# Kernel optimization log

Measured on AMD Instinct MI355X. Metric: run time of the kernel, lower is better.

## Reference

```python
import jax, jax.numpy as jnp
import numpy as np

SIGMA = 1.0


def _pairwise_max(q, fact_emb):
    # q: [B, N, D], fact_emb: [F, D]  (D = 3E)
    # Gaussian RBF kernel k(x,y) = exp(-||x-y||^2 / (2*sigma^2)), then max over F.
    q2 = jnp.sum(q * q, axis=-1, keepdims=True)            # [B, N, 1]
    f2 = jnp.sum(fact_emb * fact_emb, axis=-1)             # [F]
    qf = jnp.einsum('bnd,fd->bnf', q, fact_emb)            # [B, N, F]
    d2 = jnp.maximum(q2 + f2[None, None, :] - 2.0 * qf, 0.0)
    k = jnp.exp(-d2 / (2.0 * SIGMA ** 2))                  # [B, N, F]
    return jnp.max(k, axis=2)                              # [B, N]


def setup_inputs() -> dict:
    key = jax.random.key(0)
    ks = jax.random.split(key, 7)
    B, N, F, E = 8, 4000, 4000, 100
    return {
        'rel': jax.random.normal(ks[0], (B, E), jnp.float32),
        'arg1': jax.random.normal(ks[1], (B, E), jnp.float32),
        'arg2': jax.random.normal(ks[2], (B, E), jnp.float32),
        'fact_rel': jax.random.normal(ks[3], (F, E), jnp.float32),
        'fact_arg1': jax.random.normal(ks[4], (F, E), jnp.float32),
        'fact_arg2': jax.random.normal(ks[5], (F, E), jnp.float32),
        'entity_embeddings': jax.random.normal(ks[6], (N, E), jnp.float32),
    }


def reference(rel, arg1, arg2, fact_rel, fact_arg1, fact_arg2, entity_embeddings):
    B = rel.shape[0]
    N, E = entity_embeddings.shape
    fact_emb = jnp.concatenate([fact_rel, fact_arg1, fact_arg2], axis=1)  # [F, 3E]

    rel_b = jnp.broadcast_to(rel[:, None, :], (B, N, E))
    emb_b = jnp.broadcast_to(entity_embeddings[None, :, :], (B, N, E))

    # score_sp: query = [rel, arg1, entity]
    arg1_b = jnp.broadcast_to(arg1[:, None, :], (B, N, E))
    q_sp = jnp.concatenate([rel_b, arg1_b, emb_b], axis=2)  # [B, N, 3E]
    score_sp = _pairwise_max(q_sp, fact_emb)                # [B, N]

    # score_po: query = [rel, entity, arg2]
    arg2_b = jnp.broadcast_to(arg2[:, None, :], (B, N, E))
    q_po = jnp.concatenate([rel_b, emb_b, arg2_b], axis=2)  # [B, N, 3E]
    score_po = _pairwise_max(q_po, fact_emb)                # [B, N]

    return (score_sp, score_po)
```

## Files before the change

### kernel.cpp

```cpp
#include <hip/hip_runtime.h>
#include <math.h>

#define EDIM 100
#define KP   128
#define NF   4000
#define NN   4000
#define NB   8
#define NP   4096
#define BN   128
#define BF   64
#define FPB  4
#define NYB  16

#define CONVB (3 * NP * 16 / 256)
#define PREPB ((NP / 64) * NB)
#define E2B   ((NN + 255) / 256)

typedef __attribute__((ext_vector_type(8))) short short8;
typedef __attribute__((ext_vector_type(4))) float floatx4;

__device__ __align__(16) unsigned short g_A [NP * KP];
__device__ __align__(16) unsigned short g_B1[NP * KP];
__device__ __align__(16) unsigned short g_B2[NP * KP];
__device__ __align__(16) float g_P[2 * NB * NP];
__device__ float g_e2[NN];
__device__ float g_part[2 * NB * NYB * NP];

__device__ __forceinline__ unsigned short f2bf(float x) {
    union { float f; unsigned int u; } v; v.f = x;
    unsigned int r = v.u + 0x7FFFu + ((v.u >> 16) & 1u);
    return (unsigned short)(r >> 16);
}

__device__ __forceinline__ float row16_min(float x) {
    int i;
    i = __builtin_amdgcn_mov_dpp(__float_as_int(x), 0x140, 0xF, 0xF, false);
    x = fminf(x, __int_as_float(i));
    i = __builtin_amdgcn_mov_dpp(__float_as_int(x), 0x141, 0xF, 0xF, false);
    x = fminf(x, __int_as_float(i));
    i = __builtin_amdgcn_mov_dpp(__float_as_int(x), 0x1B, 0xF, 0xF, false);
    x = fminf(x, __int_as_float(i));
    i = __builtin_amdgcn_mov_dpp(__float_as_int(x), 0xB1, 0xF, 0xF, false);
    x = fminf(x, __int_as_float(i));
    return x;
}

__global__ void prep(const float* __restrict__ rel,  const float* __restrict__ arg1,
                     const float* __restrict__ arg2, const float* __restrict__ frel,
                     const float* __restrict__ fa1,  const float* __restrict__ fa2,
                     const float* __restrict__ ent) {
    const int bx = blockIdx.x;
    const int t  = threadIdx.x;

    if (bx < CONVB) {
        int plane = bx >> 8;
        int local = ((bx & 255) << 8) | t;
        int row = local >> 4, j = local & 15;
        const float* src = (plane == 0) ? ent : (plane == 1) ? fa1 : fa2;
        unsigned short* dst = (plane == 0) ? g_A : (plane == 1) ? g_B1 : g_B2;
        short8 o = (short8){0, 0, 0, 0, 0, 0, 0, 0};
        if (row < NF && j <= 12) {
            if (j < 12) {
                float4 v0 = *(const float4*)(src + row * EDIM + j * 8);
                float4 v1 = *(const float4*)(src + row * EDIM + j * 8 + 4);
                o[0] = (short)f2bf(v0.x); o[1] = (short)f2bf(v0.y);
                o[2] = (short)f2bf(v0.z); o[3] = (short)f2bf(v0.w);
                o[4] = (short)f2bf(v1.x); o[5] = (short)f2bf(v1.y);
                o[6] = (short)f2bf(v1.z); o[7] = (short)f2bf(v1.w);
            } else {
                float4 v0 = *(const float4*)(src + row * EDIM + 96);
                o[0] = (short)f2bf(v0.x); o[1] = (short)f2bf(v0.y);
                o[2] = (short)f2bf(v0.z); o[3] = (short)f2bf(v0.w);
            }
        }
        *(short8*)(dst + row * KP + j * 8) = o;
    } else if (bx < CONVB + PREPB) {
        int pb = bx - CONVB;
        int b   = pb >> 6;
        int fbx = pb & 63;
        int lane = t & 63;
        int wv = t >> 6;
        int fl = lane & 15;
        int kq = lane >> 4;
        int f = fbx * 64 + wv * 16 + fl;
        int fr = (f < NF) ? f : (NF - 1);

        float nf = 0.f, dr = 0.f, d1 = 0.f, d2 = 0.f, qr = 0.f, q1 = 0.f, q2 = 0.f;
        for (int i = 0; i < 25; i++) {
            int k = kq * 25 + i;
            float vr = frel[fr * EDIM + k];
            float v1 = fa1[fr * EDIM + k];
            float v2 = fa2[fr * EDIM + k];
            float rb = rel[b * EDIM + k];
            float a1 = arg1[b * EDIM + k];
            float a2 = arg2[b * EDIM + k];
            nf += vr * vr + v1 * v1 + v2 * v2;
            dr = fmaf(rb, vr, dr);
            d1 = fmaf(a1, v1, d1);
            d2 = fmaf(a2, v2, d2);
            qr = fmaf(rb, rb, qr);
            q1 = fmaf(a1, a1, q1);
            q2 = fmaf(a2, a2, q2);
        }
        nf += __shfl_xor(nf, 16); nf += __shfl_xor(nf, 32);
        dr += __shfl_xor(dr, 16); dr += __shfl_xor(dr, 32);
        d1 += __shfl_xor(d1, 16); d1 += __shfl_xor(d1, 32);
        d2 += __shfl_xor(d2, 16); d2 += __shfl_xor(d2, 32);
        qr += __shfl_xor(qr, 16); qr += __shfl_xor(qr, 32);
        q1 += __shfl_xor(q1, 16); q1 += __shfl_xor(q1, 32);
        q2 += __shfl_xor(q2, 16); q2 += __shfl_xor(q2, 32);
        if (kq == 0) {
            float psp = nf + qr + q1 - 2.f * (dr + d1);
            float ppo = nf + qr + q2 - 2.f * (dr + d2);
            if (f >= NF) { psp = __builtin_inff(); ppo = __builtin_inff(); }
            g_P[(0 * NB + b) * NP + f] = psp;
            g_P[(1 * NB + b) * NP + f] = ppo;
        }
    } else {
        int n = (bx - CONVB - PREPB) * 256 + t;
        if (n < NN) {
            const float4* ep = (const float4*)(ent + n * EDIM);
            float s = 0.f;
            #pragma unroll
            for (int i = 0; i < EDIM / 4; i++) {
                float4 v = ep[i];
                s += v.x * v.x + v.y * v.y + v.z * v.z + v.w * v.w;
            }
            g_e2[n] = s;
        }
    }
}

__global__ void __launch_bounds__(256, 2) main_kernel() {
    __shared__ float4 smem4[4352];
    float4* lA4  = smem4;
    float4* lB14 = smem4 + 2048;
    float4* lB24 = smem4 + 3072;
    float*  sPf  = (float*)(smem4 + 4096);

    const int t = threadIdx.x;
    const int n0 = blockIdx.x * BN;
    const int by = blockIdx.y;
    const int lane = t & 63;
    const int c = lane & 15;
    const int q = lane >> 4;
    const int w = t >> 6;
    const int w32 = w * 32;

    floatx4 m2[2][8][2];
    #pragma unroll
    for (int g = 0; g < 2; g++)
        #pragma unroll
        for (int b = 0; b < NB; b++)
            #pragma unroll
            for (int mt = 0; mt < 2; mt++)
                m2[g][b][mt] = (floatx4){__builtin_inff(), __builtin_inff(),
                                         __builtin_inff(), __builtin_inff()};

    const float4* gA4  = (const float4*)g_A;
    const float4* gB14 = (const float4*)g_B1;
    const float4* gB24 = (const float4*)g_B2;

    #pragma unroll
    for (int i = 0; i < 8; i++) {
        int gc = i * 256 + t;
        int rw = gc >> 4, ch = gc & 15;
        lA4[rw * 16 + (ch ^ (rw & 15))] = gA4[n0 * 16 + gc];
    }

    #pragma unroll 1
    for (int ib = 0; ib < FPB; ib++) {
        const int f0 = (by * FPB + ib) * BF;

        #pragma unroll
        for (int i = 0; i < 4; i++) {
            int gc = i * 256 + t;
            int rw = gc >> 4, ch = gc & 15;
            int sl = rw * 16 + (ch ^ (rw & 15));
            lB14[sl] = gB14[f0 * 16 + gc];
            lB24[sl] = gB24[f0 * 16 + gc];
        }
        {
            int pg = t >> 7, pb = (t >> 4) & 7, q4 = t & 15;
            ((float4*)sPf)[t] = ((const float4*)(g_P + (pg * NB + pb) * NP + f0))[q4];
        }
        __syncthreads();

        const short8* pA  = (const short8*)lA4;
        const short8* pB1 = (const short8*)lB14;
        const short8* pB2 = (const short8*)lB24;

        #pragma unroll
        for (int g = 0; g < 2; g++) {
            const short8* pB = g ? pB1 : pB2;
            floatx4 acc[2][4];
            #pragma unroll
            for (int mt = 0; mt < 2; mt++)
                #pragma unroll
                for (int ft = 0; ft < 4; ft++)
                    acc[mt][ft] = (floatx4){0.f, 0.f, 0.f, 0.f};

            #pragma unroll
            for (int s = 0; s < 4; s++) {
                const int base = s * 4 + q;
                short8 a0 = pA[(w32 + c) * 16 + (base ^ c)];
                short8 a1 = pA[(w32 + 16 + c) * 16 + (base ^ c)];
                #pragma unroll
                for (int ft = 0; ft < 4; ft++) {
                    short8 bb = pB[(ft * 16 + c) * 16 + (base ^ c)];
                    acc[0][ft] = __builtin_amdgcn_mfma_f32_16x16x32_bf16(a0, bb, acc[0][ft], 0, 0, 0);
                    acc[1][ft] = __builtin_amdgcn_mfma_f32_16x16x32_bf16(a1, bb, acc[1][ft], 0, 0, 0);
                }
            }

            #pragma unroll
            for (int b = 0; b < NB; b++) {
                const float* Pb = sPf + (g * NB + b) * 64;
                float p0 = Pb[c];
                float p1 = Pb[16 + c];
                float p2 = Pb[32 + c];
                float p3 = Pb[48 + c];
                #pragma unroll
                for (int mt = 0; mt < 2; mt++) {
                    #pragma unroll
                    for (int r = 0; r < 4; r++) {
                        float t0 = fmaf(-2.f, acc[mt][0][r], p0);
                        float t1 = fmaf(-2.f, acc[mt][1][r], p1);
                        float t2 = fmaf(-2.f, acc[mt][2][r], p2);
                        float t3 = fmaf(-2.f, acc[mt][3][r], p3);
                        float u = fminf(fminf(t0, t1), t2);
                        m2[g][b][mt][r] = fminf(fminf(u, t3), m2[g][b][mt][r]);
                    }
                }
            }
        }
        if (ib < FPB - 1) __syncthreads();
    }

    #pragma unroll
    for (int g = 0; g < 2; g++)
        #pragma unroll
        for (int b = 0; b < NB; b++)
            #pragma unroll
            for (int mt = 0; mt < 2; mt++)
                #pragma unroll
                for (int r = 0; r < 4; r++)
                    m2[g][b][mt][r] = row16_min(m2[g][b][mt][r]);

    if (c == 0) {
        #pragma unroll
        for (int g = 0; g < 2; g++)
            #pragma unroll
            for (int b = 0; b < NB; b++)
                #pragma unroll
                for (int mt = 0; mt < 2; mt++)
                    *(float4*)&g_part[((g * NB + b) * NYB + by) * NP +
                                      n0 + w32 + mt * 16 + q * 4] =
                        (float4){m2[g][b][mt][0], m2[g][b][mt][1],
                                 m2[g][b][mt][2], m2[g][b][mt][3]};
    }
}

__global__ void finalize(float* __restrict__ out) {
    int idx = blockIdx.x * 256 + threadIdx.x;
    if (idx >= 2 * NB * NN) return;
    int sb = idx / NN;
    int n = idx % NN;
    float m = __builtin_inff();
    #pragma unroll
    for (int j = 0; j < NYB; j += 2) {
        float a = g_part[(sb * NYB + j) * NP + n];
        float b = g_part[(sb * NYB + j + 1) * NP + n];
        m = fminf(m, fminf(a, b));
    }
    float d2 = fmaxf(m + g_e2[n], 0.f);
    out[idx] = expf(-0.5f * d2);
}

extern "C" void kernel_launch(void* const* d_in, const int* in_sizes, int n_in,
                              void* d_out, int out_size, void* d_ws, size_t ws_size,
                              hipStream_t stream) {
    const float* rel  = (const float*)d_in[0];
    const float* arg1 = (const float*)d_in[1];
    const float* arg2 = (const float*)d_in[2];
    const float* frel = (const float*)d_in[3];
    const float* fa1  = (const float*)d_in[4];
    const float* fa2  = (const float*)d_in[5];
    const float* ent  = (const float*)d_in[6];
    float* out = (float*)d_out;

    prep<<<dim3(CONVB + PREPB + E2B), 256, 0, stream>>>(rel, arg1, arg2, frel, fa1, fa2, ent);
    main_kernel<<<dim3(NP / BN, NYB), 256, 0, stream>>>();
    finalize<<<(2 * NB * NN + 255) / 256, 256, 0, stream>>>(out);
}
```

Baseline: 127.4 us.

## Split query groups across grid z, keep A in registers, double-buffer B via direct LDS loads

Adds a grid z dimension so each block handles only one of the two score groups, which halves the per-thread min accumulators. The A fragments are loaded straight into registers instead of shared memory. B tiles and the P vectors are double-buffered in LDS using global_load_lds, so the next tile's load overlaps the current MFMA work. P is reordered in the prep kernel into a swizzled layout so each lane reads one float4 per batch. This doubles the block count and re-reads A per group, in exchange for lower register pressure and fewer synchronisation stalls.

```diff
diff --git a/kernel.cpp b/kernel.cpp
--- a/kernel.cpp
+++ b/kernel.cpp
@@ -19,10 +19,13 @@
 typedef __attribute__((ext_vector_type(8))) short short8;
 typedef __attribute__((ext_vector_type(4))) float floatx4;
 
+typedef const __attribute__((address_space(1))) unsigned int* gas_u32;
+typedef __attribute__((address_space(3))) unsigned int* las_u32;
+
 __device__ __align__(16) unsigned short g_A [NP * KP];
 __device__ __align__(16) unsigned short g_B1[NP * KP];
 __device__ __align__(16) unsigned short g_B2[NP * KP];
-__device__ __align__(16) float g_P[2 * NB * NP];
+__device__ __align__(16) float g_P2[2 * 64 * 512];
 __device__ float g_e2[NN];
 __device__ float g_part[2 * NB * NYB * NP];
 
@@ -113,8 +116,12 @@
             float psp = nf + qr + q1 - 2.f * (dr + d1);
             float ppo = nf + qr + q2 - 2.f * (dr + d2);
             if (f >= NF) { psp = __builtin_inff(); ppo = __builtin_inff(); }
-            g_P[(0 * NB + b) * NP + f] = psp;
-            g_P[(1 * NB + b) * NP + f] = ppo;
+            int fblk = f >> 6;
+            int cc = f & 15;
+            int ft = (f & 63) >> 4;
+            int chunk = cc * 8 + (b ^ (cc & 7));
+            g_P2[(0 * 64 + fblk) * 512 + chunk * 4 + ft] = psp;
+            g_P2[(1 * 64 + fblk) * 512 + chunk * 4 + ft] = ppo;
         }
     } else {
         int n = (bx - CONVB - PREPB) * 256 + t;
@@ -132,132 +139,118 @@
 }
 
 __global__ void __launch_bounds__(256, 2) main_kernel() {
-    __shared__ float4 smem4[4352];
-    float4* lA4  = smem4;
-    float4* lB14 = smem4 + 2048;
-    float4* lB24 = smem4 + 3072;
-    float*  sPf  = (float*)(smem4 + 4096);
+    __shared__ __align__(16) unsigned short sB[2][BF * 128];
+    __shared__ __align__(16) float sP[2][512];
 
     const int t = threadIdx.x;
     const int n0 = blockIdx.x * BN;
     const int by = blockIdx.y;
+    const int g  = blockIdx.z;
     const int lane = t & 63;
     const int c = lane & 15;
     const int q = lane >> 4;
     const int w = t >> 6;
     const int w32 = w * 32;
 
-    floatx4 m2[2][8][2];
-    #pragma unroll
-    for (int g = 0; g < 2; g++)
-        #pragma unroll
-        for (int b = 0; b < NB; b++)
-            #pragma unroll
-            for (int mt = 0; mt < 2; mt++)
-                m2[g][b][mt] = (floatx4){__builtin_inff(), __builtin_inff(),
-                                         __builtin_inff(), __builtin_inff()};
-
-    const float4* gA4  = (const float4*)g_A;
-    const float4* gB14 = (const float4*)g_B1;
-    const float4* gB24 = (const float4*)g_B2;
-
-    #pragma unroll
-    for (int i = 0; i < 8; i++) {
-        int gc = i * 256 + t;
-        int rw = gc >> 4, ch = gc & 15;
-        lA4[rw * 16 + (ch ^ (rw & 15))] = gA4[n0 * 16 + gc];
-    }
+    const unsigned short* gB = g ? g_B1 : g_B2;
+
+    short8 afrag[2][4];
+    #pragma unroll
+    for (int mt = 0; mt < 2; mt++)
+        #pragma unroll
+        for (int s = 0; s < 4; s++)
+            afrag[mt][s] = *(const short8*)(g_A + (n0 + w32 + mt * 16 + c) * KP + (s * 4 + q) * 8);
+
+    floatx4 m2[NB][2];
+    #pragma unroll
+    for (int b = 0; b < NB; b++)
+        #pragma unroll
+        for (int mt = 0; mt < 2; mt++)
+            m2[b][mt] = (floatx4){__builtin_inff(), __builtin_inff(),
+                                  __builtin_inff(), __builtin_inff()};
+
+    auto stage = [&](int buf, int fb) {
+        const int f0r = fb * BF;
+        #pragma unroll
+        for (int j = 0; j < 4; j++) {
+            int ck = (w * 4 + j) * 64 + lane;
+            int rw = ck >> 4, ch = ck & 15;
+            int src = (f0r + rw) * 16 + (ch ^ (rw & 15));
+            __builtin_amdgcn_global_load_lds(
+                (gas_u32)(gB + src * 8),
+                (las_u32)(&sB[buf][(w * 4 + j) * 512]),
+                16, 0, 0);
+        }
+        if (w < 2)
+            __builtin_amdgcn_global_load_lds(
+                (gas_u32)(g_P2 + (g * 64 + fb) * 512 + w * 256 + lane * 4),
+                (las_u32)(&sP[buf][w * 256]),
+                16, 0, 0);
+    };
+
+    stage(0, by * FPB);
+    __syncthreads();
 
     #pragma unroll 1
     for (int ib = 0; ib < FPB; ib++) {
-        const int f0 = (by * FPB + ib) * BF;
-
-        #pragma unroll
-        for (int i = 0; i < 4; i++) {
-            int gc = i * 256 + t;
-            int rw = gc >> 4, ch = gc & 15;
-            int sl = rw * 16 + (ch ^ (rw & 15));
-            lB14[sl] = gB14[f0 * 16 + gc];
-            lB24[sl] = gB24[f0 * 16 + gc];
-        }
-        {
-            int pg = t >> 7, pb = (t >> 4) & 7, q4 = t & 15;
-            ((float4*)sPf)[t] = ((const float4*)(g_P + (pg * NB + pb) * NP + f0))[q4];
-        }
-        __syncthreads();
-
-        const short8* pA  = (const short8*)lA4;
-        const short8* pB1 = (const short8*)lB14;
-        const short8* pB2 = (const short8*)lB24;
-
-        #pragma unroll
-        for (int g = 0; g < 2; g++) {
-            const short8* pB = g ? pB1 : pB2;
-            floatx4 acc[2][4];
+        const int cur = ib & 1;
+        if (ib + 1 < FPB) stage(cur ^ 1, by * FPB + ib + 1);
+
+        const short8* pB = (const short8*)sB[cur];
+        floatx4 acc[2][4];
+        #pragma unroll
+        for (int mt = 0; mt < 2; mt++)
+            #pragma unroll
+            for (int ft = 0; ft < 4; ft++)
+                acc[mt][ft] = (floatx4){0.f, 0.f, 0.f, 0.f};
+
+        #pragma unroll
+        for (int s = 0; s < 4; s++) {
+            const int base = s * 4 + q;
+            #pragma unroll
+            for (int ft = 0; ft < 4; ft++) {
+                short8 bb = pB[(ft * 16 + c) * 16 + (base ^ c)];
+                acc[0][ft] = __builtin_amdgcn_mfma_f32_16x16x32_bf16(afrag[0][s], bb, acc[0][ft], 0, 0, 0);
+                acc[1][ft] = __builtin_amdgcn_mfma_f32_16x16x32_bf16(afrag[1][s], bb, acc[1][ft], 0, 0, 0);
+            }
+        }
+
+        const float* Pf = sP[cur];
+        #pragma unroll
+        for (int b = 0; b < NB; b++) {
+            floatx4 p = *(const floatx4*)(Pf + (c * 8 + (b ^ (c & 7))) * 4);
+            #pragma unroll
+            for (int mt = 0; mt < 2; mt++) {
+                #pragma unroll
+                for (int r = 0; r < 4; r++) {
+                    float t0 = fmaf(-2.f, acc[mt][0][r], p[0]);
+                    float t1 = fmaf(-2.f, acc[mt][1][r], p[1]);
+                    float t2 = fmaf(-2.f, acc[mt][2][r], p[2]);
+                    float t3 = fmaf(-2.f, acc[mt][3][r], p[3]);
+                    float u = fminf(fminf(t0, t1), t2);
+                    m2[b][mt][r] = fminf(fminf(u, t3), m2[b][mt][r]);
+                }
+            }
+        }
+        if (ib + 1 < FPB) __syncthreads();
+    }
+
+    #pragma unroll
+    for (int b = 0; b < NB; b++)
+        #pragma unroll
+        for (int mt = 0; mt < 2; mt++)
+            #pragma unroll
+            for (int r = 0; r < 4; r++)
+                m2[b][mt][r] = row16_min(m2[b][mt][r]);
+
+    if (c == 0) {
+        #pragma unroll
+        for (int b = 0; b < NB; b++)
             #pragma unroll
             for (int mt = 0; mt < 2; mt++)
-                #pragma unroll
-                for (int ft = 0; ft < 4; ft++)
-                    acc[mt][ft] = (floatx4){0.f, 0.f, 0.f, 0.f};
-
-            #pragma unroll
-            for (int s = 0; s < 4; s++) {
-                const int base = s * 4 + q;
-                short8 a0 = pA[(w32 + c) * 16 + (base ^ c)];
-                short8 a1 = pA[(w32 + 16 + c) * 16 + (base ^ c)];
-                #pragma unroll
-                for (int ft = 0; ft < 4; ft++) {
-                    short8 bb = pB[(ft * 16 + c) * 16 + (base ^ c)];
-                    acc[0][ft] = __builtin_amdgcn_mfma_f32_16x16x32_bf16(a0, bb, acc[0][ft], 0, 0, 0);
-                    acc[1][ft] = __builtin_amdgcn_mfma_f32_16x16x32_bf16(a1, bb, acc[1][ft], 0, 0, 0);
-                }
-            }
-
-            #pragma unroll
-            for (int b = 0; b < NB; b++) {
-                const float* Pb = sPf + (g * NB + b) * 64;
-                float p0 = Pb[c];
-                float p1 = Pb[16 + c];
-                float p2 = Pb[32 + c];
-                float p3 = Pb[48 + c];
-                #pragma unroll
-                for (int mt = 0; mt < 2; mt++) {
-                    #pragma unroll
-                    for (int r = 0; r < 4; r++) {
-                        float t0 = fmaf(-2.f, acc[mt][0][r], p0);
-                        float t1 = fmaf(-2.f, acc[mt][1][r], p1);
-                        float t2 = fmaf(-2.f, acc[mt][2][r], p2);
-                        float t3 = fmaf(-2.f, acc[mt][3][r], p3);
-                        float u = fminf(fminf(t0, t1), t2);
-                        m2[g][b][mt][r] = fminf(fminf(u, t3), m2[g][b][mt][r]);
-                    }
-                }
-            }
-        }
-        if (ib < FPB - 1) __syncthreads();
-    }
-
-    #pragma unroll
-    for (int g = 0; g < 2; g++)
-        #pragma unroll
-        for (int b = 0; b < NB; b++)
-            #pragma unroll
-            for (int mt = 0; mt < 2; mt++)
-                #pragma unroll
-                for (int r = 0; r < 4; r++)
-                    m2[g][b][mt][r] = row16_min(m2[g][b][mt][r]);
-
-    if (c == 0) {
-        #pragma unroll
-        for (int g = 0; g < 2; g++)
-            #pragma unroll
-            for (int b = 0; b < NB; b++)
-                #pragma unroll
-                for (int mt = 0; mt < 2; mt++)
-                    *(float4*)&g_part[((g * NB + b) * NYB + by) * NP +
-                                      n0 + w32 + mt * 16 + q * 4] =
-                        (float4){m2[g][b][mt][0], m2[g][b][mt][1],
-                                 m2[g][b][mt][2], m2[g][b][mt][3]};
+                *(float4*)&g_part[((g * NB + b) * NYB + by) * NP +
+                                  n0 + w32 + mt * 16 + q * 4] =
+                    (float4){m2[b][mt][0], m2[b][mt][1], m2[b][mt][2], m2[b][mt][3]};
     }
 }
 
@@ -290,6 +283,6 @@
     float* out = (float*)d_out;
 
     prep<<<dim3(CONVB + PREPB + E2B), 256, 0, stream>>>(rel, arg1, arg2, frel, fa1, fa2, ent);
-    main_kernel<<<dim3(NP / BN, NYB), 256, 0, stream>>>();
+    main_kernel<<<dim3(NP / BN, NYB, 2), 256, 0, stream>>>();
     finalize<<<(2 * NB * NN + 255) / 256, 256, 0, stream>>>(out);
 }
```

Result: faster. 112.5 us (-11.7%).
